# Performance work log

Hardware: AMD Instinct MI355X
Metric: run time of the kernel (lower is better)

Reference implementation:

```python
import jax, jax.numpy as jnp
import numpy as np

EMBED_DIM = 1024
NUM_HEADS = 16
HEAD_DIM = EMBED_DIM // NUM_HEADS
SCALE = HEAD_DIM ** -0.5


def setup_inputs() -> dict:
    key = jax.random.key(0)
    k1, k2, k3, k4 = jax.random.split(key, 4)
    B, N, D = 2, 2048, EMBED_DIM
    x = jax.random.normal(k1, (B, N, D), dtype=jnp.float32)
    # nn.Linear weights stored as [out, in]; we keep [in, out] for x @ W
    w_qkv = jax.random.normal(k2, (D, 3 * D), dtype=jnp.float32) * (D ** -0.5)
    w_proj = jax.random.normal(k3, (D, D), dtype=jnp.float32) * (D ** -0.5)
    b_proj = jax.random.normal(k4, (D,), dtype=jnp.float32) * 0.01
    return {"x": x, "w_qkv": w_qkv, "w_proj": w_proj, "b_proj": b_proj}


def reference(x, w_qkv, w_proj, b_proj):
    B, N, D = x.shape
    H, Hd = NUM_HEADS, HEAD_DIM
    qkv = x @ w_qkv  # [B, N, 3D]
    q, k, v = jnp.split(qkv, 3, axis=-1)
    # [B, N, D] -> [B, H, N, Hd]
    split_heads = lambda t: t.reshape(B, N, H, Hd).transpose(0, 2, 1, 3)
    q, k, v = split_heads(q), split_heads(k), split_heads(v)
    a = jnp.einsum("bhqd,bhkd->bhqk", q, k) * SCALE
    a = jax.nn.softmax(a, axis=-1)
    out = jnp.einsum("bhqk,bhkd->bhqd", a, v)
    out = out.transpose(0, 2, 1, 3).reshape(B, N, D)
    return out @ w_proj + b_proj
```

## Files before the change

### kernel.cpp

```cpp
#include <hip/hip_runtime.h>
#include <stdint.h>

typedef __attribute__((ext_vector_type(8))) short bf16x8;
typedef __attribute__((ext_vector_type(4))) float f32x4;
typedef __attribute__((ext_vector_type(4))) float float4v;
typedef __attribute__((ext_vector_type(8))) unsigned short u16x8;

#define DEV __device__ __forceinline__

DEV unsigned short f2bf(float f) {
    union { float f; uint32_t u; } v; v.f = f;
    uint32_t u = v.u;
    return (unsigned short)((u + 0x7FFFu + ((u >> 16) & 1u)) >> 16);
}

DEV unsigned int cvt_pk_bf16(float lo, float hi) {
    unsigned int r;
    asm("v_cvt_pk_bf16_f32 %0, %1, %2" : "=v"(r) : "v"(lo), "v"(hi));
    return r;
}

#if __has_builtin(__builtin_amdgcn_global_load_lds)
#define HAVE_GLDS 1
typedef const unsigned char __attribute__((address_space(1)))* as1p;
typedef unsigned char __attribute__((address_space(3)))* as3p;
DEV void gload16(const unsigned short* g, unsigned short* l) {
    __builtin_amdgcn_global_load_lds((as1p)(const void*)g, (as3p)(void*)l, 16, 0, 0);
}
#else
#define HAVE_GLDS 0
#endif

__global__ void k_cvt_x(const float* __restrict__ x, unsigned short* __restrict__ xb, int n4) {
    int i = blockIdx.x * blockDim.x + threadIdx.x;
    if (i >= n4) return;
    float4v v = *(const float4v*)(x + (size_t)i * 4);
    union { unsigned short s[4]; uint64_t q; } o;
    o.s[0] = f2bf(v[0]); o.s[1] = f2bf(v[1]); o.s[2] = f2bf(v[2]); o.s[3] = f2bf(v[3]);
    *(uint64_t*)(xb + (size_t)i * 4) = o.q;
}

__global__ void k_cvt_tr_w(const float* __restrict__ w, unsigned short* __restrict__ wt,
                           int R, int C) {
    __shared__ alignas(16) unsigned short tile[64][65];
    const int t = threadIdx.x;
    const int tr = blockIdx.y * 64, tc = blockIdx.x * 64;
#pragma unroll
    for (int p = 0; p < 4; ++p) {
        int r = p * 16 + (t >> 4);
        int c = (t & 15) * 4;
        float4v v = *(const float4v*)(w + (size_t)(tr + r) * C + tc + c);
#pragma unroll
        for (int j = 0; j < 4; ++j) tile[r][c + j] = f2bf(v[j]);
    }
    __syncthreads();
#pragma unroll
    for (int p = 0; p < 2; ++p) {
        int r2 = p * 32 + (t >> 3);
        int k0 = (t & 7) * 8;
        u16x8 o;
#pragma unroll
        for (int j = 0; j < 8; ++j) o[j] = tile[k0 + j][r2];
        *(u16x8*)(wt + (size_t)(tc + r2) * R + tr + k0) = o;
    }
}

template <int OUT_BF16>
__global__ __launch_bounds__(256)
void k_gemm_bt(const unsigned short* __restrict__ A,
               const unsigned short* __restrict__ Bt,
               void* __restrict__ Cp, const float* __restrict__ bias,
               unsigned short* __restrict__ vt_out,
               int M, int N, int K) {
    __shared__ alignas(16) unsigned short lA[128 * 64];
    __shared__ alignas(16) unsigned short lB[128 * 64];
    const int t = threadIdx.x;
    const int w = t >> 6, l = t & 63;
    const int l15 = l & 15, l4 = l >> 4;
    const int wm = (w >> 1) * 64, wn = (w & 1) * 64;
    const size_t bm = (size_t)blockIdx.y * 128, bn = (size_t)blockIdx.x * 128;

    int offA[4][2], offB[4][2];
#pragma unroll
    for (int f = 0; f < 4; ++f) {
        const int ra = wm + f * 16 + l15;
        const int rb = wn + f * 16 + l15;
#pragma unroll
        for (int kc = 0; kc < 2; ++kc) {
            offA[f][kc] = ra * 64 + (((kc * 4 + l4) ^ (ra & 7)) << 3);
            offB[f][kc] = rb * 64 + (((kc * 4 + l4) ^ (rb & 7)) << 3);
        }
    }

#if HAVE_GLDS
    const int srow8 = l >> 3;
    const int scol  = (l & 7) ^ srow8;
    const unsigned short* gA = A  + (bm + w * 32 + srow8) * (size_t)K + scol * 8;
    const unsigned short* gB = Bt + (bn + w * 32 + srow8) * (size_t)K + scol * 8;
    unsigned short* dA = lA + (w * 32) * 64;
    unsigned short* dB = lB + (w * 32) * 64;
#else
    const int srow = t >> 3, sslot = t & 7;
    const int swoff = srow * 64 + ((sslot ^ (srow & 7)) << 3);
    const unsigned short* pA = A + (bm + srow) * (size_t)K + sslot * 8;
    const unsigned short* pB = Bt + (bn + srow) * (size_t)K + sslot * 8;
#endif

    const f32x4 zf = {0.f, 0.f, 0.f, 0.f};
    f32x4 acc[4][4];
#pragma unroll
    for (int i = 0; i < 4; ++i)
#pragma unroll
        for (int j = 0; j < 4; ++j) acc[i][j] = zf;

    for (int kt = 0; kt < K; kt += 64) {
#if HAVE_GLDS
        __syncthreads();
#pragma unroll
        for (int i = 0; i < 4; ++i) {
            gload16(gA + (size_t)i * 8 * K + kt, dA + i * 8 * 64);
            gload16(gB + (size_t)i * 8 * K + kt, dB + i * 8 * 64);
        }
        __syncthreads();
#else
        bf16x8 ra[4], rb[4];
#pragma unroll
        for (int p = 0; p < 4; ++p) {
            ra[p] = *(const bf16x8*)(pA + (size_t)p * 32 * K + kt);
            rb[p] = *(const bf16x8*)(pB + (size_t)p * 32 * K + kt);
        }
        __syncthreads();
#pragma unroll
        for (int p = 0; p < 4; ++p) {
            *(bf16x8*)(lA + p * 32 * 64 + swoff) = ra[p];
            *(bf16x8*)(lB + p * 32 * 64 + swoff) = rb[p];
        }
        __syncthreads();
#endif
#pragma unroll
        for (int kc = 0; kc < 2; ++kc) {
            bf16x8 af[4], bfr[4];
#pragma unroll
            for (int f = 0; f < 4; ++f) af[f] = *(const bf16x8*)(lA + offA[f][kc]);
#pragma unroll
            for (int f = 0; f < 4; ++f) bfr[f] = *(const bf16x8*)(lB + offB[f][kc]);
#pragma unroll
            for (int mf = 0; mf < 4; ++mf)
#pragma unroll
                for (int nf = 0; nf < 4; ++nf)
                    acc[mf][nf] = __builtin_amdgcn_mfma_f32_16x16x32_bf16(
                        af[mf], bfr[nf], acc[mf][nf], 0, 0, 0);
        }
    }

    if (OUT_BF16) {
        if (vt_out && bn >= 2048) {
            const int bb = (int)(bm >> 11);
            const int n0 = (int)(bm & 2047) + wm + l4 * 4;
#pragma unroll
            for (int nf = 0; nf < 4; ++nf) {
                const int d = (int)(bn - 2048) + wn + nf * 16 + l15;
                unsigned short* vrow = vt_out + ((size_t)(bb * 16 + (d >> 6)) * 64 + (d & 63)) * 2048;
#pragma unroll
                for (int mf = 0; mf < 4; ++mf) {
                    union { unsigned short s[4]; uint64_t q; } u;
#pragma unroll
                    for (int j = 0; j < 4; ++j) u.s[j] = f2bf(acc[mf][nf][j]);
                    *(uint64_t*)(vrow + n0 + mf * 16) = u.q;
                }
            }
        } else {
            unsigned short* C = (unsigned short*)Cp;
#pragma unroll
            for (int mf = 0; mf < 4; ++mf)
#pragma unroll
                for (int nf = 0; nf < 4; ++nf) {
                    const size_t row = bm + wm + mf * 16 + l4 * 4;
                    const size_t col = bn + wn + nf * 16 + l15;
#pragma unroll
                    for (int j = 0; j < 4; ++j)
                        C[(row + j) * (size_t)N + col] = f2bf(acc[mf][nf][j]);
                }
        }
    } else {
        float* C = (float*)Cp;
#pragma unroll
        for (int nf = 0; nf < 4; ++nf) {
            const size_t col = bn + wn + nf * 16 + l15;
            const float bv = bias[col];
#pragma unroll
            for (int mf = 0; mf < 4; ++mf) {
                const size_t row = bm + wm + mf * 16 + l4 * 4;
#pragma unroll
                for (int j = 0; j < 4; ++j)
                    C[(row + j) * (size_t)N + col] = acc[mf][nf][j] + bv;
            }
        }
    }
}

__global__ __launch_bounds__(256, 4)
void k_attn(const unsigned short* __restrict__ qkv, const unsigned short* __restrict__ vt,
            unsigned short* __restrict__ attn_out) {
    __shared__ alignas(16) unsigned short lK[2][64 * 64];
    __shared__ alignas(16) unsigned short lV[2][64 * 64];
    __shared__ alignas(16) unsigned short lP[4][16 * 64];
    const int t = threadIdx.x, w = t >> 6, l = t & 63;
    const int l15 = l & 15, l4 = l >> 4;
    const int bh = blockIdx.y, b = bh >> 4, h = bh & 15;
    const int qb = blockIdx.x * 64;
    const float QSCALE = 0.18033688011112042f;

    const unsigned short* qptr =
        qkv + (size_t)(b * 2048 + qb + w * 16 + l15) * 3072 + h * 64 + l4 * 8;
    const bf16x8 aq0 = *(const bf16x8*)(qptr);
    const bf16x8 aq1 = *(const bf16x8*)(qptr + 32);

#if HAVE_GLDS
    const int gr = l >> 3;
    const int gs = (l & 7) ^ gr;
    const unsigned short* gK = qkv + (size_t)(b * 2048 + w * 16 + gr) * 3072 + 1024 + h * 64 + gs * 8;
    const unsigned short* gV = vt + (size_t)(bh * 64 + w * 16 + gr) * 2048 + gs * 8;
#else
    const int srow = t >> 3, sslot = t & 7;
    const int swoff = srow * 64 + ((sslot ^ (srow & 7)) << 3);
    const unsigned short* kptr = qkv + (size_t)(b * 2048 + srow) * 3072 + 1024 + h * 64 + sslot * 8;
    const unsigned short* vptr = vt + (size_t)(bh * 64 + srow) * 2048 + sslot * 8;
#endif

    int offK[4][2];
#pragma unroll
    for (int nf = 0; nf < 4; ++nf) {
        const int r = nf * 16 + l15;
#pragma unroll
        for (int kc = 0; kc < 2; ++kc)
            offK[nf][kc] = r * 64 + (((kc * 4 + l4) ^ (r & 7)) << 3);
    }
    int offPw[4];
#pragma unroll
    for (int nf = 0; nf < 4; ++nf) {
        const int c = nf * 16 + l4 * 4;
        offPw[nf] = l15 * 64 + (((c >> 3) ^ (l15 & 7)) << 3) + (c & 7);
    }

    const f32x4 zf = {0.f, 0.f, 0.f, 0.f};
    f32x4 o[4];
#pragma unroll
    for (int df = 0; df < 4; ++df) o[df] = zf;
    f32x4 accl = zf;
    float m_run = -1e30f;
    unsigned short* Pw = &lP[w][0];
    const bf16x8 ones8 = {(short)0x3F80, (short)0x3F80, (short)0x3F80, (short)0x3F80,
                          (short)0x3F80, (short)0x3F80, (short)0x3F80, (short)0x3F80};

#if HAVE_GLDS
#pragma unroll
    for (int i = 0; i < 2; ++i) {
        gload16(gK + (size_t)i * 8 * 3072, &lK[0][(w * 16 + i * 8) * 64]);
        gload16(gV + (size_t)i * 8 * 2048, &lV[0][(w * 16 + i * 8) * 64]);
    }
    __syncthreads();
#else
    {
        bf16x8 rk[2], rv[2];
#pragma unroll
        for (int p = 0; p < 2; ++p) {
            rk[p] = *(const bf16x8*)(kptr + (size_t)(p * 32) * 3072);
            rv[p] = *(const bf16x8*)(vptr + (size_t)(p * 32) * 2048);
        }
#pragma unroll
        for (int p = 0; p < 2; ++p) {
            *(bf16x8*)(&lK[0][0] + p * 32 * 64 + swoff) = rk[p];
            *(bf16x8*)(&lV[0][0] + p * 32 * 64 + swoff) = rv[p];
        }
        __syncthreads();
    }
#endif

#pragma unroll 2
    for (int kt = 0; kt < 2048; kt += 64) {
        const int cur = (kt >> 6) & 1;
        const unsigned short* K = &lK[cur][0];
        const unsigned short* V = &lV[cur][0];
        const bool more = (kt + 64) < 2048;

#if HAVE_GLDS
        if (more) {
#pragma unroll
            for (int i = 0; i < 2; ++i) {
                gload16(gK + (size_t)(kt + 64 + i * 8) * 3072, &lK[cur ^ 1][(w * 16 + i * 8) * 64]);
                gload16(gV + (size_t)i * 8 * 2048 + kt + 64,   &lV[cur ^ 1][(w * 16 + i * 8) * 64]);
            }
        }
#else
        bf16x8 rk[2], rv[2];
        if (more) {
#pragma unroll
            for (int p = 0; p < 2; ++p) {
                rk[p] = *(const bf16x8*)(kptr + (size_t)(kt + 64 + p * 32) * 3072);
                rv[p] = *(const bf16x8*)(vptr + (size_t)(p * 32) * 2048 + kt + 64);
            }
        }
#endif

        f32x4 s[4];
        __builtin_amdgcn_s_setprio(1);
#pragma unroll
        for (int nf = 0; nf < 4; ++nf) {
            const bf16x8 kf0 = *(const bf16x8*)(K + offK[nf][0]);
            const bf16x8 kf1 = *(const bf16x8*)(K + offK[nf][1]);
            f32x4 a = zf;
            a = __builtin_amdgcn_mfma_f32_16x16x32_bf16(kf0, aq0, a, 0, 0, 0);
            a = __builtin_amdgcn_mfma_f32_16x16x32_bf16(kf1, aq1, a, 0, 0, 0);
            s[nf] = a;
        }
        __builtin_amdgcn_s_setprio(0);

        float mx = fmaxf(fmaxf(s[0][0], s[0][1]), s[0][2]);
        mx = fmaxf(fmaxf(mx, s[0][3]), s[1][0]);
        mx = fmaxf(fmaxf(mx, s[1][1]), s[1][2]);
        mx = fmaxf(fmaxf(mx, s[1][3]), s[2][0]);
        mx = fmaxf(fmaxf(mx, s[2][1]), s[2][2]);
        mx = fmaxf(fmaxf(mx, s[2][3]), s[3][0]);
        mx = fmaxf(fmaxf(mx, s[3][1]), s[3][2]);
        mx = fmaxf(mx, s[3][3]);
        mx = fmaxf(mx, __shfl_xor(mx, 16));
        mx = fmaxf(mx, __shfl_xor(mx, 32));
        mx *= QSCALE;

        if (!__all(mx <= m_run + 8.0f)) {
            const float mn = fmaxf(m_run, mx);
            const float alpha = exp2f(m_run - mn);
            m_run = mn;
            const float a0 = __shfl(alpha, l4 * 4 + 0);
            const float a1 = __shfl(alpha, l4 * 4 + 1);
            const float a2 = __shfl(alpha, l4 * 4 + 2);
            const float a3 = __shfl(alpha, l4 * 4 + 3);
#pragma unroll
            for (int df = 0; df < 4; ++df) {
                o[df][0] *= a0; o[df][1] *= a1; o[df][2] *= a2; o[df][3] *= a3;
            }
            accl[0] *= a0; accl[1] *= a1; accl[2] *= a2; accl[3] *= a3;
        }

#pragma unroll
        for (int nf = 0; nf < 4; ++nf) {
            const float p0 = exp2f(fmaf(s[nf][0], QSCALE, -m_run));
            const float p1 = exp2f(fmaf(s[nf][1], QSCALE, -m_run));
            const float p2 = exp2f(fmaf(s[nf][2], QSCALE, -m_run));
            const float p3 = exp2f(fmaf(s[nf][3], QSCALE, -m_run));
            union { unsigned int d[2]; uint64_t q; } u;
            u.d[0] = cvt_pk_bf16(p0, p1);
            u.d[1] = cvt_pk_bf16(p2, p3);
            *(uint64_t*)(Pw + offPw[nf]) = u.q;
        }

        const bf16x8 ap0 = *(const bf16x8*)(Pw + l15 * 64 + ((l4 ^ (l15 & 7)) << 3));
        const bf16x8 ap1 = *(const bf16x8*)(Pw + l15 * 64 + (((4 + l4) ^ (l15 & 7)) << 3));
        __builtin_amdgcn_s_setprio(1);
        accl = __builtin_amdgcn_mfma_f32_16x16x32_bf16(ap0, ones8, accl, 0, 0, 0);
        accl = __builtin_amdgcn_mfma_f32_16x16x32_bf16(ap1, ones8, accl, 0, 0, 0);
#pragma unroll
        for (int df = 0; df < 4; ++df) {
            const int r = df * 16 + l15;
            const bf16x8 bv0 = *(const bf16x8*)(V + r * 64 + ((l4 ^ (r & 7)) << 3));
            const bf16x8 bv1 = *(const bf16x8*)(V + r * 64 + (((4 + l4) ^ (r & 7)) << 3));
            o[df] = __builtin_amdgcn_mfma_f32_16x16x32_bf16(ap0, bv0, o[df], 0, 0, 0);
            o[df] = __builtin_amdgcn_mfma_f32_16x16x32_bf16(ap1, bv1, o[df], 0, 0, 0);
        }
        __builtin_amdgcn_s_setprio(0);

#if !HAVE_GLDS
        if (more) {
#pragma unroll
            for (int p = 0; p < 2; ++p) {
                *(bf16x8*)(&lK[cur ^ 1][0] + p * 32 * 64 + swoff) = rk[p];
                *(bf16x8*)(&lV[cur ^ 1][0] + p * 32 * 64 + swoff) = rv[p];
            }
        }
#endif
        __syncthreads();
    }

    const float r0 = 1.0f / accl[0];
    const float r1 = 1.0f / accl[1];
    const float r2 = 1.0f / accl[2];
    const float r3 = 1.0f / accl[3];
    const int rowb = b * 2048 + qb + w * 16 + l4 * 4;
#pragma unroll
    for (int df = 0; df < 4; ++df) {
        const int d = df * 16 + l15;
        attn_out[(size_t)(rowb + 0) * 1024 + h * 64 + d] = f2bf(o[df][0] * r0);
        attn_out[(size_t)(rowb + 1) * 1024 + h * 64 + d] = f2bf(o[df][1] * r1);
        attn_out[(size_t)(rowb + 2) * 1024 + h * 64 + d] = f2bf(o[df][2] * r2);
        attn_out[(size_t)(rowb + 3) * 1024 + h * 64 + d] = f2bf(o[df][3] * r3);
    }
}

extern "C" void kernel_launch(void* const* d_in, const int* in_sizes, int n_in,
                              void* d_out, int out_size, void* d_ws, size_t ws_size,
                              hipStream_t stream) {
    const float* x      = (const float*)d_in[0];
    const float* w_qkv  = (const float*)d_in[1];
    const float* w_proj = (const float*)d_in[2];
    const float* b_proj = (const float*)d_in[3];
    float* out = (float*)d_out;

    char* ws = (char*)d_ws;
    unsigned short* xb     = (unsigned short*)(ws + 0);
    unsigned short* wqkvT  = (unsigned short*)(ws + 8388608);
    unsigned short* wprojT = (unsigned short*)(ws + 14680064);
    unsigned short* qkv    = (unsigned short*)(ws + 16777216);
    unsigned short* vt     = (unsigned short*)(ws + 41943040);
    unsigned short* attn   = (unsigned short*)(ws + 50331648);

    k_cvt_x<<<dim3(4096), dim3(256), 0, stream>>>(x, xb, 4096 * 1024 / 4);
    k_cvt_tr_w<<<dim3(48, 16), dim3(256), 0, stream>>>(w_qkv, wqkvT, 1024, 3072);
    k_cvt_tr_w<<<dim3(16, 16), dim3(256), 0, stream>>>(w_proj, wprojT, 1024, 1024);
    k_gemm_bt<1><<<dim3(24, 32), dim3(256), 0, stream>>>(xb, wqkvT, (void*)qkv, (const float*)nullptr, vt, 4096, 3072, 1024);
    k_attn<<<dim3(32, 32), dim3(256), 0, stream>>>(qkv, vt, attn);
    k_gemm_bt<0><<<dim3(8, 32), dim3(256), 0, stream>>>(attn, wprojT, (void*)out, b_proj, (unsigned short*)nullptr, 4096, 1024, 1024);
}
```

Before: 139.1 us.

## Halve projection GEMM N-tile and drop async LDS loads in attention

Templates the GEMM on the N tile width and launches the output projection with 64-wide tiles, doubling its grid from 256 to 512 blocks so more CUs have work. Separately, the attention kernel's global_load_lds direct-to-LDS path for K/V is removed, so it always uses register-staged loads that are written to LDS after the compute. Smaller tiles give less operand reuse per block, and register staging uses more VGPRs but lets the loads overlap with the MFMA work.

```diff
diff --git a/kernel.cpp b/kernel.cpp
--- a/kernel.cpp
+++ b/kernel.cpp
@@ -65,40 +65,45 @@
     }
 }
 
-template <int OUT_BF16>
+template <int OUT_BF16, int BN>
 __global__ __launch_bounds__(256)
 void k_gemm_bt(const unsigned short* __restrict__ A,
                const unsigned short* __restrict__ Bt,
                void* __restrict__ Cp, const float* __restrict__ bias,
                unsigned short* __restrict__ vt_out,
                int M, int N, int K) {
+    constexpr int NFR = BN / 32;
     __shared__ alignas(16) unsigned short lA[128 * 64];
-    __shared__ alignas(16) unsigned short lB[128 * 64];
+    __shared__ alignas(16) unsigned short lB[BN * 64];
     const int t = threadIdx.x;
     const int w = t >> 6, l = t & 63;
     const int l15 = l & 15, l4 = l >> 4;
-    const int wm = (w >> 1) * 64, wn = (w & 1) * 64;
-    const size_t bm = (size_t)blockIdx.y * 128, bn = (size_t)blockIdx.x * 128;
-
-    int offA[4][2], offB[4][2];
+    const int wm = (w >> 1) * 64, wn = (w & 1) * (BN / 2);
+    const size_t bm = (size_t)blockIdx.y * 128, bn = (size_t)blockIdx.x * BN;
+
+    int offA[4][2], offB[NFR][2];
 #pragma unroll
     for (int f = 0; f < 4; ++f) {
         const int ra = wm + f * 16 + l15;
+#pragma unroll
+        for (int kc = 0; kc < 2; ++kc)
+            offA[f][kc] = ra * 64 + (((kc * 4 + l4) ^ (ra & 7)) << 3);
+    }
+#pragma unroll
+    for (int f = 0; f < NFR; ++f) {
         const int rb = wn + f * 16 + l15;
 #pragma unroll
-        for (int kc = 0; kc < 2; ++kc) {
-            offA[f][kc] = ra * 64 + (((kc * 4 + l4) ^ (ra & 7)) << 3);
+        for (int kc = 0; kc < 2; ++kc)
             offB[f][kc] = rb * 64 + (((kc * 4 + l4) ^ (rb & 7)) << 3);
-        }
     }
 
 #if HAVE_GLDS
     const int srow8 = l >> 3;
     const int scol  = (l & 7) ^ srow8;
     const unsigned short* gA = A  + (bm + w * 32 + srow8) * (size_t)K + scol * 8;
-    const unsigned short* gB = Bt + (bn + w * 32 + srow8) * (size_t)K + scol * 8;
+    const unsigned short* gB = Bt + (bn + w * (BN / 4) + srow8) * (size_t)K + scol * 8;
     unsigned short* dA = lA + (w * 32) * 64;
-    unsigned short* dB = lB + (w * 32) * 64;
+    unsigned short* dB = lB + (w * (BN / 4)) * 64;
 #else
     const int srow = t >> 3, sslot = t & 7;
     const int swoff = srow * 64 + ((sslot ^ (srow & 7)) << 3);
@@ -107,47 +112,50 @@
 #endif
 
     const f32x4 zf = {0.f, 0.f, 0.f, 0.f};
-    f32x4 acc[4][4];
+    f32x4 acc[4][NFR];
 #pragma unroll
     for (int i = 0; i < 4; ++i)
 #pragma unroll
-        for (int j = 0; j < 4; ++j) acc[i][j] = zf;
+        for (int j = 0; j < NFR; ++j) acc[i][j] = zf;
 
     for (int kt = 0; kt < K; kt += 64) {
 #if HAVE_GLDS
         __syncthreads();
 #pragma unroll
-        for (int i = 0; i < 4; ++i) {
+        for (int i = 0; i < 4; ++i)
             gload16(gA + (size_t)i * 8 * K + kt, dA + i * 8 * 64);
+#pragma unroll
+        for (int i = 0; i < BN / 32; ++i)
             gload16(gB + (size_t)i * 8 * K + kt, dB + i * 8 * 64);
-        }
         __syncthreads();
 #else
-        bf16x8 ra[4], rb[4];
-#pragma unroll
-        for (int p = 0; p < 4; ++p) {
+        bf16x8 ra[4], rb[BN / 32];
+#pragma unroll
+        for (int p = 0; p < 4; ++p)
             ra[p] = *(const bf16x8*)(pA + (size_t)p * 32 * K + kt);
+#pragma unroll
+        for (int p = 0; p < BN / 32; ++p)
             rb[p] = *(const bf16x8*)(pB + (size_t)p * 32 * K + kt);
-        }
-        __syncthreads();
-#pragma unroll
-        for (int p = 0; p < 4; ++p) {
+        __syncthreads();
+#pragma unroll
+        for (int p = 0; p < 4; ++p)
             *(bf16x8*)(lA + p * 32 * 64 + swoff) = ra[p];
+#pragma unroll
+        for (int p = 0; p < BN / 32; ++p)
             *(bf16x8*)(lB + p * 32 * 64 + swoff) = rb[p];
-        }
         __syncthreads();
 #endif
 #pragma unroll
         for (int kc = 0; kc < 2; ++kc) {
-            bf16x8 af[4], bfr[4];
+            bf16x8 af[4], bfr[NFR];
 #pragma unroll
             for (int f = 0; f < 4; ++f) af[f] = *(const bf16x8*)(lA + offA[f][kc]);
 #pragma unroll
-            for (int f = 0; f < 4; ++f) bfr[f] = *(const bf16x8*)(lB + offB[f][kc]);
+            for (int f = 0; f < NFR; ++f) bfr[f] = *(const bf16x8*)(lB + offB[f][kc]);
 #pragma unroll
             for (int mf = 0; mf < 4; ++mf)
 #pragma unroll
-                for (int nf = 0; nf < 4; ++nf)
+                for (int nf = 0; nf < NFR; ++nf)
                     acc[mf][nf] = __builtin_amdgcn_mfma_f32_16x16x32_bf16(
                         af[mf], bfr[nf], acc[mf][nf], 0, 0, 0);
         }
@@ -158,7 +166,7 @@
             const int bb = (int)(bm >> 11);
             const int n0 = (int)(bm & 2047) + wm + l4 * 4;
 #pragma unroll
-            for (int nf = 0; nf < 4; ++nf) {
+            for (int nf = 0; nf < NFR; ++nf) {
                 const int d = (int)(bn - 2048) + wn + nf * 16 + l15;
                 unsigned short* vrow = vt_out + ((size_t)(bb * 16 + (d >> 6)) * 64 + (d & 63)) * 2048;
 #pragma unroll
@@ -174,7 +182,7 @@
 #pragma unroll
             for (int mf = 0; mf < 4; ++mf)
 #pragma unroll
-                for (int nf = 0; nf < 4; ++nf) {
+                for (int nf = 0; nf < NFR; ++nf) {
                     const size_t row = bm + wm + mf * 16 + l4 * 4;
                     const size_t col = bn + wn + nf * 16 + l15;
 #pragma unroll
@@ -185,7 +193,7 @@
     } else {
         float* C = (float*)Cp;
 #pragma unroll
-        for (int nf = 0; nf < 4; ++nf) {
+        for (int nf = 0; nf < NFR; ++nf) {
             const size_t col = bn + wn + nf * 16 + l15;
             const float bv = bias[col];
 #pragma unroll
@@ -216,17 +224,10 @@
     const bf16x8 aq0 = *(const bf16x8*)(qptr);
     const bf16x8 aq1 = *(const bf16x8*)(qptr + 32);
 
-#if HAVE_GLDS
-    const int gr = l >> 3;
-    const int gs = (l & 7) ^ gr;
-    const unsigned short* gK = qkv + (size_t)(b * 2048 + w * 16 + gr) * 3072 + 1024 + h * 64 + gs * 8;
-    const unsigned short* gV = vt + (size_t)(bh * 64 + w * 16 + gr) * 2048 + gs * 8;
-#else
     const int srow = t >> 3, sslot = t & 7;
     const int swoff = srow * 64 + ((sslot ^ (srow & 7)) << 3);
     const unsigned short* kptr = qkv + (size_t)(b * 2048 + srow) * 3072 + 1024 + h * 64 + sslot * 8;
     const unsigned short* vptr = vt + (size_t)(bh * 64 + srow) * 2048 + sslot * 8;
-#endif
 
     int offK[4][2];
 #pragma unroll
@@ -253,14 +254,6 @@
     const bf16x8 ones8 = {(short)0x3F80, (short)0x3F80, (short)0x3F80, (short)0x3F80,
                           (short)0x3F80, (short)0x3F80, (short)0x3F80, (short)0x3F80};
 
-#if HAVE_GLDS
-#pragma unroll
-    for (int i = 0; i < 2; ++i) {
-        gload16(gK + (size_t)i * 8 * 3072, &lK[0][(w * 16 + i * 8) * 64]);
-        gload16(gV + (size_t)i * 8 * 2048, &lV[0][(w * 16 + i * 8) * 64]);
-    }
-    __syncthreads();
-#else
     {
         bf16x8 rk[2], rv[2];
 #pragma unroll
@@ -275,25 +268,15 @@
         }
         __syncthreads();
     }
-#endif
 
 #pragma unroll 2
     for (int kt = 0; kt < 2048; kt += 64) {
         const int cur = (kt >> 6) & 1;
         const unsigned short* K = &lK[cur][0];
         const unsigned short* V = &lV[cur][0];
+
+        bf16x8 rk[2], rv[2];
         const bool more = (kt + 64) < 2048;
-
-#if HAVE_GLDS
-        if (more) {
-#pragma unroll
-            for (int i = 0; i < 2; ++i) {
-                gload16(gK + (size_t)(kt + 64 + i * 8) * 3072, &lK[cur ^ 1][(w * 16 + i * 8) * 64]);
-                gload16(gV + (size_t)i * 8 * 2048 + kt + 64,   &lV[cur ^ 1][(w * 16 + i * 8) * 64]);
-            }
-        }
-#else
-        bf16x8 rk[2], rv[2];
         if (more) {
 #pragma unroll
             for (int p = 0; p < 2; ++p) {
@@ -301,7 +284,6 @@
                 rv[p] = *(const bf16x8*)(vptr + (size_t)(p * 32) * 2048 + kt + 64);
             }
         }
-#endif
 
         f32x4 s[4];
         __builtin_amdgcn_s_setprio(1);
@@ -370,7 +352,6 @@
         }
         __builtin_amdgcn_s_setprio(0);
 
-#if !HAVE_GLDS
         if (more) {
 #pragma unroll
             for (int p = 0; p < 2; ++p) {
@@ -378,7 +359,6 @@
                 *(bf16x8*)(&lV[cur ^ 1][0] + p * 32 * 64 + swoff) = rv[p];
             }
         }
-#endif
         __syncthreads();
     }
 
@@ -417,7 +397,7 @@
     k_cvt_x<<<dim3(4096), dim3(256), 0, stream>>>(x, xb, 4096 * 1024 / 4);
     k_cvt_tr_w<<<dim3(48, 16), dim3(256), 0, stream>>>(w_qkv, wqkvT, 1024, 3072);
     k_cvt_tr_w<<<dim3(16, 16), dim3(256), 0, stream>>>(w_proj, wprojT, 1024, 1024);
-    k_gemm_bt<1><<<dim3(24, 32), dim3(256), 0, stream>>>(xb, wqkvT, (void*)qkv, (const float*)nullptr, vt, 4096, 3072, 1024);
+    k_gemm_bt<1, 128><<<dim3(24, 32), dim3(256), 0, stream>>>(xb, wqkvT, (void*)qkv, (const float*)nullptr, vt, 4096, 3072, 1024);
     k_attn<<<dim3(32, 32), dim3(256), 0, stream>>>(qkv, vt, attn);
-    k_gemm_bt<0><<<dim3(8, 32), dim3(256), 0, stream>>>(attn, wprojT, (void*)out, b_proj, (unsigned short*)nullptr, 4096, 1024, 1024);
-}
+    k_gemm_bt<0, 64><<<dim3(16, 32), dim3(256), 0, stream>>>(attn, wprojT, (void*)out, b_proj, (unsigned short*)nullptr, 4096, 1024, 1024);
+}
```

Result: faster. 133.2 us (-4.2%).
